# Kernel tuning notes

Hardware: AMD Instinct MI355X
Metric: run time of the kernel (lower is better)

## Reference

```python
import jax, jax.numpy as jnp
import numpy as np

D_MODEL, N_HEADS, D_K, D_V, D_FF, N_LAYERS = 512, 8, 64, 64, 2048, 6
NEG = -1e9
EPS = 1e-5


def layernorm(x):
    # nn.LayerNorm(d_model) created fresh each call: weight=1, bias=0
    mu = jnp.mean(x, axis=-1, keepdims=True)
    var = jnp.var(x, axis=-1, keepdims=True)
    return (x - mu) * jax.lax.rsqrt(var + EPS)


def sinusoidal_pe(seq_len, d_model, dtype=jnp.float32):
    pos = np.arange(seq_len)[:, None].astype(np.float64)
    div = np.exp(np.arange(0, d_model, 2).astype(np.float64) * (-np.log(10000.0) / d_model))
    pe = np.zeros((seq_len, d_model))
    pe[:, 0::2] = np.sin(pos * div)
    pe[:, 1::2] = np.cos(pos * div)
    return jnp.asarray(pe, dtype=dtype)


def mha(q_in, k_in, v_in, mask, Wq, Wk, Wv, Wo):
    # q_in: [B,Lq,D]; k_in/v_in: [B,Lk,D]; mask: [B,Lq,Lk] bool (True = masked)
    B, Lq, _ = q_in.shape
    Lk = k_in.shape[1]
    Q = (q_in @ Wq).reshape(B, Lq, N_HEADS, D_K).transpose(0, 2, 1, 3)
    K = (k_in @ Wk).reshape(B, Lk, N_HEADS, D_K).transpose(0, 2, 1, 3)
    V = (v_in @ Wv).reshape(B, Lk, N_HEADS, D_V).transpose(0, 2, 1, 3)
    scores = jnp.einsum('bhqd,bhkd->bhqk', Q, K) / jnp.sqrt(jnp.asarray(D_K, q_in.dtype))
    scores = jnp.where(mask[:, None, :, :], jnp.asarray(NEG, scores.dtype), scores)
    attn = jax.nn.softmax(scores, axis=-1)
    ctx = jnp.einsum('bhqk,bhkd->bhqd', attn, V)
    ctx = ctx.transpose(0, 2, 1, 3).reshape(B, Lq, N_HEADS * D_V)
    return layernorm(ctx @ Wo + q_in)


def setup_inputs() -> dict:
    key = jax.random.key(0)
    ks = jax.random.split(key, 16)
    B, T, S, V = 8, 1024, 1024, 32000
    s = 0.02
    inp = {
        'dec_inputs': jax.random.randint(ks[0], (B, T), 0, V),
        'enc_inputs': jax.random.randint(ks[1], (B, S), 0, V),
        'enc_outputs': jax.random.normal(ks[2], (B, S, D_MODEL), jnp.float32),
        'emb': jax.random.normal(ks[3], (V, D_MODEL), jnp.float32) * s,
        'Wq_self': jax.random.normal(ks[4], (N_LAYERS, D_MODEL, N_HEADS * D_K), jnp.float32) * s,
        'Wk_self': jax.random.normal(ks[5], (N_LAYERS, D_MODEL, N_HEADS * D_K), jnp.float32) * s,
        'Wv_self': jax.random.normal(ks[6], (N_LAYERS, D_MODEL, N_HEADS * D_V), jnp.float32) * s,
        'Wo_self': jax.random.normal(ks[7], (N_LAYERS, N_HEADS * D_V, D_MODEL), jnp.float32) * s,
        'Wq_cross': jax.random.normal(ks[8], (N_LAYERS, D_MODEL, N_HEADS * D_K), jnp.float32) * s,
        'Wk_cross': jax.random.normal(ks[9], (N_LAYERS, D_MODEL, N_HEADS * D_K), jnp.float32) * s,
        'Wv_cross': jax.random.normal(ks[10], (N_LAYERS, D_MODEL, N_HEADS * D_V), jnp.float32) * s,
        'Wo_cross': jax.random.normal(ks[11], (N_LAYERS, N_HEADS * D_V, D_MODEL), jnp.float32) * s,
        'W1': jax.random.normal(ks[12], (N_LAYERS, D_MODEL, D_FF), jnp.float32) * s,
        'W2': jax.random.normal(ks[13], (N_LAYERS, D_FF, D_MODEL), jnp.float32) * s,
    }
    return inp


def reference(dec_inputs, enc_inputs, enc_outputs, emb, Wq_self, Wk_self, Wv_self, Wo_self,
              Wq_cross, Wk_cross, Wv_cross, Wo_cross, W1, W2):
    B, T = dec_inputs.shape
    S = enc_inputs.shape[1]
    # embedding with padding_idx=0 (row 0 forced to zero)
    emb_eff = emb.at[0].set(0.0)
    x = emb_eff[dec_inputs] + sinusoidal_pe(T, D_MODEL, emb.dtype)[None, :, :]
    # masks: True = masked
    pad_self = (dec_inputs == 0)[:, None, :]                       # [B,1,T]
    causal = jnp.triu(jnp.ones((T, T), bool), k=1)[None, :, :]     # [1,T,T]
    self_mask = pad_self | causal                                  # [B,T,T]
    enc_mask = jnp.broadcast_to((enc_inputs == 0)[:, None, :], (B, T, S))

    def layer(x, p):
        wqs, wks, wvs, wos, wqc, wkc, wvc, woc, w1, w2 = p
        x = mha(x, x, x, self_mask, wqs, wks, wvs, wos)
        x = mha(x, enc_outputs, enc_outputs, enc_mask, wqc, wkc, wvc, woc)
        h = jax.nn.relu(x @ w1) @ w2
        return layernorm(h + x), None

    params = (Wq_self, Wk_self, Wv_self, Wo_self, Wq_cross, Wk_cross, Wv_cross, Wo_cross, W1, W2)
    x, _ = jax.lax.scan(layer, x, params)
    return x
```

## Files before the change

kernel.cpp:

```cpp
#include <hip/hip_runtime.h>
#include <hip/hip_bf16.h>

#define DMODEL 512
#define NH     8
#define DHEAD  64
#define DFF    2048
#define NLAYER 6
#define BB     8
#define TT     1024
#define NTOK   (BB*TT)
#define ACTE   ((size_t)NTOK*DMODEL)

#define QSCALE 0.18033688011112042f

typedef __bf16  bf16x8  __attribute__((ext_vector_type(8)));
typedef float   float4v __attribute__((ext_vector_type(4)));
typedef short   short4v __attribute__((ext_vector_type(4)));
typedef short   short8v __attribute__((ext_vector_type(8)));

__device__ __forceinline__ unsigned short f2bf(float f) {
    __hip_bfloat16 h = __float2bfloat16(f);
    return *reinterpret_cast<unsigned short*>(&h);
}

__device__ __forceinline__ float exp2_fast(float x) {
    float r;
    asm("v_exp_f32 %0, %1\n\ts_nop 0" : "=v"(r) : "v"(x));
    return r;
}

__device__ __forceinline__ void gl_lds16(const void* g, void* l) {
    __builtin_amdgcn_global_load_lds((const __attribute__((address_space(1))) void*)g,
                                     (__attribute__((address_space(3))) void*)l, 16, 0, 0);
}

struct Tr8Args {
    const float* src[8];
    unsigned short* dst[8];
    int dstL[8];
    int rowOff[8];
};
__global__ __launch_bounds__(256) void transpose8_kernel(Tr8Args a)
{
    __shared__ float tile[64][65];
    const int type = blockIdx.z / 6, lyr = blockIdx.z % 6;
    const float* src = a.src[type] + (size_t)lyr * 512 * 512;
    unsigned short* dst = a.dst[type] + (size_t)lyr * a.dstL[type];
    const int rowOff = a.rowOff[type];
    const int k0 = blockIdx.x * 64, n0 = blockIdx.y * 64;
    const int tid = threadIdx.x;
#pragma unroll
    for (int rep = 0; rep < 16; ++rep) {
        int idx = rep * 256 + tid;
        int r = idx >> 6, c = idx & 63;
        tile[r][c] = src[(size_t)(k0 + r) * 512 + n0 + c];
    }
    __syncthreads();
#pragma unroll
    for (int rep = 0; rep < 16; ++rep) {
        int idx = rep * 256 + tid;
        int r = idx >> 6, c = idx & 63;
        dst[(size_t)(rowOff + n0 + r) * 512 + k0 + c] = f2bf(tile[c][r]);
    }
}

__global__ __launch_bounds__(256) void transpose_conv_kernel(
    const float* __restrict__ W, unsigned short* __restrict__ Wt, int K, int N,
    size_t dstL, int rowOff)
{
    __shared__ float tile[64][65];
    const float* src = W + (size_t)blockIdx.z * K * N;
    unsigned short* dst = Wt + (size_t)blockIdx.z * dstL;
    const int k0 = blockIdx.x * 64, n0 = blockIdx.y * 64;
    const int tid = threadIdx.x;
#pragma unroll
    for (int rep = 0; rep < 16; ++rep) {
        int idx = rep * 256 + tid;
        int r = idx >> 6, c = idx & 63;
        tile[r][c] = src[(size_t)(k0 + r) * N + n0 + c];
    }
    __syncthreads();
#pragma unroll
    for (int rep = 0; rep < 16; ++rep) {
        int idx = rep * 256 + tid;
        int r = idx >> 6, c = idx & 63;
        dst[(size_t)(rowOff + n0 + r) * K + k0 + c] = f2bf(tile[c][r]);
    }
}

__global__ __launch_bounds__(256) void conv_bf16_kernel(
    const float* __restrict__ in, unsigned short* __restrict__ o)
{
    int i = (blockIdx.x * 256 + threadIdx.x) * 4;
    float4v v = *(const float4v*)(in + i);
    short4v w;
    w[0] = (short)f2bf(v[0]); w[1] = (short)f2bf(v[1]);
    w[2] = (short)f2bf(v[2]); w[3] = (short)f2bf(v[3]);
    *(short4v*)(o + i) = w;
}

__global__ __launch_bounds__(256) void embed_kernel(
    const int* __restrict__ dec, const float* __restrict__ emb,
    unsigned short* __restrict__ xb)
{
    const int row = blockIdx.x;
    const int t = row & (TT - 1);
    const int tid = threadIdx.x;
    const int tok = dec[row];
#pragma unroll
    for (int rep = 0; rep < 2; ++rep) {
        int c = tid + rep * 256;
        float e = (tok != 0) ? emb[(size_t)tok * DMODEL + c] : 0.f;
        int j = c >> 1;
        float freq = __expf(-(float)(2 * j) * (9.210340371976184f / 512.f));
        float ang = (float)t * freq;
        float pe = (c & 1) ? cosf(ang) : sinf(ang);
        xb[(size_t)row * DMODEL + c] = f2bf(e + pe);
    }
}

__global__ __launch_bounds__(256) void add_ln2(
    const float* __restrict__ t, unsigned short* __restrict__ xb,
    float* __restrict__ xout)
{
    const int lane = threadIdx.x & 63;
    const int row = blockIdx.x * 4 + (threadIdx.x >> 6);
    const size_t idx = (size_t)row * DMODEL + lane * 8;
    float4v t0 = *(const float4v*)(t + idx);
    float4v t1 = *(const float4v*)(t + idx + 4);
    float4v u0 = *(const float4v*)(t + ACTE + idx);
    float4v u1 = *(const float4v*)(t + ACTE + idx + 4);
    bf16x8 rb = *(const bf16x8*)(xb + idx);
    float v[8];
#pragma unroll
    for (int k = 0; k < 4; ++k) {
        v[k] = t0[k] + u0[k] + (float)rb[k];
        v[4 + k] = t1[k] + u1[k] + (float)rb[4 + k];
    }
    float s = 0.f, sq = 0.f;
#pragma unroll
    for (int k = 0; k < 8; ++k) { s += v[k]; sq += v[k] * v[k]; }
#pragma unroll
    for (int o = 1; o < 64; o <<= 1) { s += __shfl_xor(s, o); sq += __shfl_xor(sq, o); }
    float mu = s * (1.f / 512.f);
    float var = sq * (1.f / 512.f) - mu * mu;
    float rstd = rsqrtf(var + 1e-5f);
    if (xout) {
        float4v y0, y1;
#pragma unroll
        for (int k = 0; k < 4; ++k) { y0[k] = (v[k] - mu) * rstd; y1[k] = (v[4 + k] - mu) * rstd; }
        *(float4v*)(xout + idx) = y0;
        *(float4v*)(xout + idx + 4) = y1;
    } else {
        short8v w;
#pragma unroll
        for (int k = 0; k < 8; ++k) w[k] = (short)f2bf((v[k] - mu) * rstd);
        *(short8v*)(xb + idx) = w;
    }
}

template <int EPI, int SPLITK = 1>
__global__ __launch_bounds__(256) void gemm_bt(
    const unsigned short* __restrict__ A,
    const unsigned short* __restrict__ Bt,
    float* __restrict__ Cf,
    unsigned short* __restrict__ Cb,
    int M, int N, int K)
{
    __shared__ __attribute__((aligned(16))) short As[128 * 32];
    __shared__ __attribute__((aligned(16))) short Bs[128 * 32];
    const int tid = threadIdx.x;
    const int lane = tid & 63, wv = tid >> 6;
    const int quad = lane >> 4, l15 = lane & 15;
    const int m0 = blockIdx.x * 128, n0 = blockIdx.y * 128;
    const int wm = wv & 1, wn = wv >> 1;

    float4v acc[4][4];
#pragma unroll
    for (int i = 0; i < 4; ++i)
#pragma unroll
        for (int j = 0; j < 4; ++j) acc[i][j] = (float4v){0.f, 0.f, 0.f, 0.f};

    const int Kc = K / SPLITK;
    const int kbeg = (SPLITK > 1) ? (int)blockIdx.z * Kc : 0;
    for (int k0 = kbeg; k0 < kbeg + Kc; k0 += 32) {
#pragma unroll
        for (int i = 0; i < 2; ++i) {
            const int inst = wv * 2 + i;
            const int row = inst * 16 + (lane >> 2);
            const int cb = (lane & 3) ^ ((row >> 1) & 3);
            gl_lds16(A + (size_t)(m0 + row) * K + k0 + cb * 8, (char*)As + inst * 1024);
            gl_lds16(Bt + (size_t)(n0 + row) * K + k0 + cb * 8, (char*)Bs + inst * 1024);
        }
        __syncthreads();
        bf16x8 a[4], b[4];
#pragma unroll
        for (int i = 0; i < 4; ++i) {
            const int r = wm * 64 + i * 16 + l15;
            const int st = quad ^ ((r >> 1) & 3);
            a[i] = *(const bf16x8*)&As[r * 32 + st * 8];
        }
#pragma unroll
        for (int j = 0; j < 4; ++j) {
            const int r = wn * 64 + j * 16 + l15;
            const int st = quad ^ ((r >> 1) & 3);
            b[j] = *(const bf16x8*)&Bs[r * 32 + st * 8];
        }
#pragma unroll
        for (int i = 0; i < 4; ++i)
#pragma unroll
            for (int j = 0; j < 4; ++j)
                acc[i][j] = __builtin_amdgcn_mfma_f32_16x16x32_bf16(a[i], b[j], acc[i][j], 0, 0, 0);
        __syncthreads();
    }

    const size_t zoff = (SPLITK > 1) ? (size_t)blockIdx.z * ACTE : 0;
#pragma unroll
    for (int i = 0; i < 4; ++i) {
        const int row_base = m0 + wm * 64 + i * 16 + quad * 4;
#pragma unroll
        for (int j = 0; j < 4; ++j) {
            const int col = n0 + wn * 64 + j * 16 + l15;
#pragma unroll
            for (int r = 0; r < 4; ++r) {
                const int row = row_base + r;
                const float v = acc[i][j][r];
                if (EPI == 0) {
                    Cf[zoff + (size_t)row * N + col] = v;
                } else if (EPI == 1) {
                    Cb[(size_t)row * N + col] = f2bf(fmaxf(v, 0.f));
                } else if (EPI == 2) {
                    const int which = col >> 9;
                    const float sc = (which == 0) ? QSCALE : 1.f;
                    const int b_ = row >> 10, t = row & (TT - 1);
                    const int h = (col >> 6) & 7, d = col & 63;
                    Cb[(size_t)which * ACTE + (((size_t)(b_ * NH + h)) * TT + t) * DHEAD + d] = f2bf(v * sc);
                } else {
                    const int layer = col >> 10, which = (col >> 9) & 1;
                    const int b_ = row >> 10, t = row & (TT - 1);
                    const int h = (col >> 6) & 7, d = col & 63;
                    Cb[(size_t)(layer * 2 + which) * ACTE +
                       (((size_t)(b_ * NH + h)) * TT + t) * DHEAD + d] = f2bf(v);
                }
            }
        }
    }
}

template <bool CAUSAL>
__global__ __launch_bounds__(256, 2) void attn_kernel(
    const unsigned short* __restrict__ Q,
    const unsigned short* __restrict__ Kb,
    const unsigned short* __restrict__ Vb,
    const int* __restrict__ tokens,
    unsigned short* __restrict__ ctx)
{
    __shared__ __attribute__((aligned(16))) short Ks[2][64 * 64];
    __shared__ __attribute__((aligned(16))) short Vt[2][64 * 64];
    __shared__ __attribute__((aligned(16))) short Pl[2][4][16 * 72];
    __shared__ __attribute__((aligned(16))) float alph[2][4][16];

    const int tid = threadIdx.x, lane = tid & 63, wv = tid >> 6;
    const int quad = lane >> 4, l15 = lane & 15;
    const int p = blockIdx.x;
    const int bh = blockIdx.y;
    const int b = bh >> 3, h = bh & 7;
    const size_t kvbase = (size_t)bh * TT * DHEAD;

    const int qt0 = p;
    const int qt1 = CAUSAL ? (15 - p) : (p + 8);
    const int qg0 = qt0 * 64 + wv * 16 + l15;
    const int qg1 = qt1 * 64 + wv * 16 + l15;

    const bf16x8 qa0 = *(const bf16x8*)&Q[kvbase + (size_t)qg0 * DHEAD + quad * 8];
    const bf16x8 qa1 = *(const bf16x8*)&Q[kvbase + (size_t)qg0 * DHEAD + 32 + quad * 8];
    const bf16x8 qb0 = *(const bf16x8*)&Q[kvbase + (size_t)qg1 * DHEAD + quad * 8];
    const bf16x8 qb1 = *(const bf16x8*)&Q[kvbase + (size_t)qg1 * DHEAD + 32 + quad * 8];

    float4v O0[4], O1[4];
#pragma unroll
    for (int j = 0; j < 4; ++j) { O0[j] = (float4v){0.f,0.f,0.f,0.f}; O1[j] = (float4v){0.f,0.f,0.f,0.f}; }
    float m0_ = -INFINITY, l0_ = 0.f, m1_ = -INFINITY, l1_ = 0.f;

    const int key0 = (lane & 31) * 2;
    const int d0 = (lane >> 5) * 8 + wv * 16;
    auto stageK = [&](int kt_, int buf) {
#pragma unroll
        for (int i = 0; i < 2; ++i) {
            const int inst = wv * 2 + i;
            const int row = inst * 8 + (lane >> 3);
            const int cb = (lane & 7) ^ (row & 7);
            gl_lds16(Kb + kvbase + (size_t)(kt_ * 64 + row) * DHEAD + cb * 8,
                     (char*)Ks[buf] + inst * 1024);
        }
    };
    auto loadV = [&](int kt_, short8v& r0, short8v& r1) {
        const unsigned short* vp = Vb + kvbase + (size_t)(kt_ * 64 + key0) * DHEAD + d0;
        r0 = *(const short8v*)vp;
        r1 = *(const short8v*)(vp + DHEAD);
    };
    auto writeV = [&](int buf, const short8v& r0, const short8v& r1) {
        const int kc = key0 >> 3, ko = key0 & 7;
#pragma unroll
        for (int j = 0; j < 8; ++j) {
            const int d = d0 + j;
            unsigned pk = (unsigned)(unsigned short)r0[j] |
                          ((unsigned)(unsigned short)r1[j] << 16);
            *(unsigned*)&Vt[buf][d * 64 + ((kc ^ (d & 7)) << 3) + ko] = pk;
        }
    };

    int kt = 0;
    bf16x8 kf[4][2], vf[4][2];

    auto process = [&](int ch, const bf16x8& qf0, const bf16x8& qf1, int qg,
                       float& m, float& l, float4v* O, unsigned long long kbits) {
        float4v st[4];
#pragma unroll
        for (int i = 0; i < 4; ++i) {
            float4v z = (float4v){0.f, 0.f, 0.f, 0.f};
            z = __builtin_amdgcn_mfma_f32_16x16x32_bf16(kf[i][0], qf0, z, 0, 0, 0);
            z = __builtin_amdgcn_mfma_f32_16x16x32_bf16(kf[i][1], qf1, z, 0, 0, 0);
            st[i] = z;
        }
        unsigned long long mask = kbits;
        if (CAUSAL && kt * 64 + 63 > qg) {
            const int qcol = qg & 63;
            mask |= (qcol == 63) ? 0ull : (~0ull << (qcol + 1));
        }
        float sv[16], smax = -INFINITY;
#pragma unroll
        for (int i = 0; i < 4; ++i)
#pragma unroll
            for (int r = 0; r < 4; ++r) {
                const int kl = i * 16 + quad * 4 + r;
                float s = ((mask >> kl) & 1ull) ? -1e9f : st[i][r];
                sv[i * 4 + r] = s;
                smax = fmaxf(smax, s);
            }
        smax = fmaxf(smax, __shfl_xor(smax, 16));
        smax = fmaxf(smax, __shfl_xor(smax, 32));
        const float mnew = fmaxf(m, smax);
        const float alpha = exp2_fast(m - mnew);
        float tsum = 0.f;
#pragma unroll
        for (int i = 0; i < 16; ++i) { float pv = exp2_fast(sv[i] - mnew); sv[i] = pv; tsum += pv; }
        tsum += __shfl_xor(tsum, 16);
        tsum += __shfl_xor(tsum, 32);
        l = l * alpha + tsum;
        m = mnew;
#pragma unroll
        for (int i = 0; i < 4; ++i) {
            short4v pw;
#pragma unroll
            for (int r = 0; r < 4; ++r) pw[r] = (short)f2bf(sv[i * 4 + r]);
            *(short4v*)&Pl[ch][wv][l15 * 72 + i * 16 + quad * 4] = pw;
        }
        if (lane < 16) alph[ch][wv][lane] = alpha;
        const float4v aw = *(const float4v*)&alph[ch][wv][quad * 4];
        const bf16x8 p0 = *(const bf16x8*)&Pl[ch][wv][l15 * 72 + quad * 8];
        const bf16x8 p1 = *(const bf16x8*)&Pl[ch][wv][l15 * 72 + 32 + quad * 8];
#pragma unroll
        for (int j = 0; j < 4; ++j) {
            float4v o = O[j] * aw;
            o = __builtin_amdgcn_mfma_f32_16x16x32_bf16(p0, vf[j][0], o, 0, 0, 0);
            o = __builtin_amdgcn_mfma_f32_16x16x32_bf16(p1, vf[j][1], o, 0, 0, 0);
            O[j] = o;
        }
    };

    const int nkt = CAUSAL ? (qt1 + 1) : 16;

    stageK(0, 0);
    {
        short8v v0a, v0b;
        loadV(0, v0a, v0b);
        writeV(0, v0a, v0b);
    }
    int tok_cur = tokens[(size_t)b * TT + lane];
    __syncthreads();

    short8v vn0, vn1;
    int tok_next = 0;
    for (kt = 0; kt < nkt; ++kt) {
        const int cur = kt & 1, nxt = cur ^ 1;
        const bool more = (kt + 1 < nkt);
        if (more) {
            stageK(kt + 1, nxt);
            loadV(kt + 1, vn0, vn1);
            tok_next = tokens[(size_t)b * TT + (kt + 1) * 64 + lane];
        }
        const unsigned long long kbits = __ballot(tok_cur == 0);

#pragma unroll
        for (int i = 0; i < 4; ++i) {
            const int row = i * 16 + l15;
            const int s0 = quad ^ (row & 7);
            const int s1 = (4 + quad) ^ (row & 7);
            kf[i][0] = *(const bf16x8*)&Ks[cur][row * 64 + s0 * 8];
            kf[i][1] = *(const bf16x8*)&Ks[cur][row * 64 + s1 * 8];
            vf[i][0] = *(const bf16x8*)&Vt[cur][row * 64 + s0 * 8];
            vf[i][1] = *(const bf16x8*)&Vt[cur][row * 64 + s1 * 8];
        }

        if (!CAUSAL || kt <= qt0) process(0, qa0, qa1, qg0, m0_, l0_, O0, kbits);
        process(1, qb0, qb1, qg1, m1_, l1_, O1, kbits);

        if (more) {
            writeV(nxt, vn0, vn1);
            tok_cur = tok_next;
        }
        __syncthreads();
    }

    auto finalize = [&](int ch, float l, float4v* O, int qt) {
        if (lane < 16) alph[ch][wv][lane] = l;
        const float4v lw = *(const float4v*)&alph[ch][wv][quad * 4];
#pragma unroll
        for (int j = 0; j < 4; ++j)
#pragma unroll
            for (int r = 0; r < 4; ++r) {
                const int qrow = qt * 64 + wv * 16 + quad * 4 + r;
                ctx[((size_t)b * TT + qrow) * DMODEL + h * DHEAD + j * 16 + l15] =
                    f2bf(O[j][r] / lw[r]);
            }
    };
    finalize(0, l0_, O0, qt0);
    finalize(1, l1_, O1, qt1);
}

extern "C" void kernel_launch(void* const* d_in, const int* in_sizes, int n_in,
                              void* d_out, int out_size, void* d_ws, size_t ws_size,
                              hipStream_t stream)
{
    const int* dec = (const int*)d_in[0];
    const int* enc = (const int*)d_in[1];
    const float* enc_out = (const float*)d_in[2];
    const float* emb = (const float*)d_in[3];
    const float* Wq_s = (const float*)d_in[4];
    const float* Wk_s = (const float*)d_in[5];
    const float* Wv_s = (const float*)d_in[6];
    const float* Wo_s = (const float*)d_in[7];
    const float* Wq_c = (const float*)d_in[8];
    const float* Wk_c = (const float*)d_in[9];
    const float* Wv_c = (const float*)d_in[10];
    const float* Wo_c = (const float*)d_in[11];
    const float* W1 = (const float*)d_in[12];
    const float* W2 = (const float*)d_in[13];
    float* out = (float*)d_out;

    char* p = (char*)d_ws;
    auto carve = [&](size_t bytes) -> char* {
        char* r = p;
        p += (bytes + 255) & ~(size_t)255;
        return r;
    };
    unsigned short* xb   = (unsigned short*)carve(ACTE * 2);
    float* tmp1          = (float*)carve(2 * ACTE * 4);
    unsigned short* qkvb = (unsigned short*)carve(3 * ACTE * 2);
    unsigned short* ctxb = (unsigned short*)carve(ACTE * 2);
    unsigned short* encb = (unsigned short*)carve(ACTE * 2);
    unsigned short* h1   = (unsigned short*)carve((size_t)NTOK * DFF * 2);
    unsigned short* wqkvT = (unsigned short*)carve((size_t)NLAYER * 1536 * 512 * 2);
    unsigned short* woT   = (unsigned short*)carve((size_t)NLAYER * 512 * 512 * 2);
    unsigned short* wqcT  = (unsigned short*)carve((size_t)NLAYER * 512 * 512 * 2);
    unsigned short* wkvcT = (unsigned short*)carve((size_t)NLAYER * 1024 * 512 * 2);
    unsigned short* wocT  = (unsigned short*)carve((size_t)NLAYER * 512 * 512 * 2);
    unsigned short* w1T   = (unsigned short*)carve((size_t)NLAYER * 2048 * 512 * 2);
    unsigned short* w2T   = (unsigned short*)carve((size_t)NLAYER * 512 * 2048 * 2);
    const size_t used = (size_t)(p - (char*)d_ws);
    const bool pre = (used + 12 * ACTE * 2 + 256) <= ws_size;
    unsigned short* KVc = pre ? (unsigned short*)carve(12 * ACTE * 2) : nullptr;

    Tr8Args ta;
    ta.src[0] = Wq_s; ta.dst[0] = wqkvT; ta.dstL[0] = 1536 * 512; ta.rowOff[0] = 0;
    ta.src[1] = Wk_s; ta.dst[1] = wqkvT; ta.dstL[1] = 1536 * 512; ta.rowOff[1] = 512;
    ta.src[2] = Wv_s; ta.dst[2] = wqkvT; ta.dstL[2] = 1536 * 512; ta.rowOff[2] = 1024;
    ta.src[3] = Wo_s; ta.dst[3] = woT;   ta.dstL[3] = 512 * 512;  ta.rowOff[3] = 0;
    ta.src[4] = Wq_c; ta.dst[4] = wqcT;  ta.dstL[4] = 512 * 512;  ta.rowOff[4] = 0;
    ta.src[5] = Wk_c; ta.dst[5] = wkvcT; ta.dstL[5] = 1024 * 512; ta.rowOff[5] = 0;
    ta.src[6] = Wv_c; ta.dst[6] = wkvcT; ta.dstL[6] = 1024 * 512; ta.rowOff[6] = 512;
    ta.src[7] = Wo_c; ta.dst[7] = wocT;  ta.dstL[7] = 512 * 512;  ta.rowOff[7] = 0;
    transpose8_kernel<<<dim3(8, 8, 48), 256, 0, stream>>>(ta);
    transpose_conv_kernel<<<dim3(8, 32, NLAYER), 256, 0, stream>>>(W1, w1T, 512, 2048, (size_t)2048 * 512, 0);
    transpose_conv_kernel<<<dim3(32, 8, NLAYER), 256, 0, stream>>>(W2, w2T, 2048, 512, (size_t)512 * 2048, 0);
    conv_bf16_kernel<<<(int)(ACTE / 1024), 256, 0, stream>>>(enc_out, encb);
    embed_kernel<<<NTOK, 256, 0, stream>>>(dec, emb, xb);

    if (pre)
        gemm_bt<3><<<dim3(64, 48), 256, 0, stream>>>(encb, wkvcT, nullptr, KVc, NTOK, 6144, 512);

    for (int lyr = 0; lyr < NLAYER; ++lyr) {
        const unsigned short* wqkv = wqkvT + (size_t)lyr * 1536 * 512;
        const unsigned short* wo   = woT + (size_t)lyr * 512 * 512;
        const unsigned short* wqc  = wqcT + (size_t)lyr * 512 * 512;
        const unsigned short* wkvc = wkvcT + (size_t)lyr * 1024 * 512;
        const unsigned short* woc  = wocT + (size_t)lyr * 512 * 512;
        const unsigned short* w1   = w1T + (size_t)lyr * 2048 * 512;
        const unsigned short* w2   = w2T + (size_t)lyr * 512 * 2048;

        gemm_bt<2><<<dim3(64, 12), 256, 0, stream>>>(xb, wqkv, nullptr, qkvb, NTOK, 1536, 512);
        attn_kernel<true><<<dim3(8, BB * NH), 256, 0, stream>>>(
            qkvb, qkvb + ACTE, qkvb + 2 * ACTE, dec, ctxb);
        gemm_bt<0, 2><<<dim3(64, 4, 2), 256, 0, stream>>>(ctxb, wo, tmp1, nullptr, NTOK, 512, 512);
        add_ln2<<<NTOK / 4, 256, 0, stream>>>(tmp1, xb, nullptr);

        gemm_bt<2><<<dim3(64, 4), 256, 0, stream>>>(xb, wqc, nullptr, qkvb, NTOK, 512, 512);
        const unsigned short* Kc;
        if (pre) {
            Kc = KVc + (size_t)lyr * 2 * ACTE;
        } else {
            gemm_bt<2><<<dim3(64, 8), 256, 0, stream>>>(encb, wkvc, nullptr, qkvb + ACTE, NTOK, 1024, 512);
            Kc = qkvb + ACTE;
        }
        attn_kernel<false><<<dim3(8, BB * NH), 256, 0, stream>>>(
            qkvb, Kc, Kc + ACTE, enc, ctxb);
        gemm_bt<0, 2><<<dim3(64, 4, 2), 256, 0, stream>>>(ctxb, woc, tmp1, nullptr, NTOK, 512, 512);
        add_ln2<<<NTOK / 4, 256, 0, stream>>>(tmp1, xb, nullptr);

        gemm_bt<1><<<dim3(64, 16), 256, 0, stream>>>(xb, w1, nullptr, h1, NTOK, 2048, 512);
        gemm_bt<0, 2><<<dim3(64, 4, 2), 256, 0, stream>>>(h1, w2, tmp1, nullptr, NTOK, 512, 2048);
        add_ln2<<<NTOK / 4, 256, 0, stream>>>(tmp1, xb, (lyr == NLAYER - 1) ? out : nullptr);
    }
    (void)in_sizes; (void)n_in; (void)out_size;
}
```

Baseline: 1.647 ms.

## Add lazy softmax rescaling, MFMA priority hints, and swapped attention grid order

The attention kernel now skips the running-max update and O rescale unless some lane's new max exceeds the old one by more than a threshold, as in FA4-style lazy rescaling. It also raises wave priority around the MFMA blocks, widens the P LDS stride to 80, and replaces the final division with a reciprocal multiply. The grid is transposed so that batch-head varies fastest across blocks. These changes are meant to cut exp and rescale ALU work and to change scheduling and cache locality. In exchange they add a wave-wide vote and bound the overflow risk by the threshold.

Result: faster. 1.610 ms (-2.2%).

```diff
diff --git a/kernel.cpp b/kernel.cpp
--- a/kernel.cpp
+++ b/kernel.cpp
@@ -13,6 +13,10 @@
 
 #define QSCALE 0.18033688011112042f
 
+#define RESCALE_THR 8.0f
+
+#define PST 80
+
 typedef __bf16  bf16x8  __attribute__((ext_vector_type(8)));
 typedef float   float4v __attribute__((ext_vector_type(4)));
 typedef short   short4v __attribute__((ext_vector_type(4)));
@@ -21,12 +25,6 @@
 __device__ __forceinline__ unsigned short f2bf(float f) {
     __hip_bfloat16 h = __float2bfloat16(f);
     return *reinterpret_cast<unsigned short*>(&h);
-}
-
-__device__ __forceinline__ float exp2_fast(float x) {
-    float r;
-    asm("v_exp_f32 %0, %1\n\ts_nop 0" : "=v"(r) : "v"(x));
-    return r;
 }
 
 __device__ __forceinline__ void gl_lds16(const void* g, void* l) {
@@ -257,13 +255,13 @@
 {
     __shared__ __attribute__((aligned(16))) short Ks[2][64 * 64];
     __shared__ __attribute__((aligned(16))) short Vt[2][64 * 64];
-    __shared__ __attribute__((aligned(16))) short Pl[2][4][16 * 72];
+    __shared__ __attribute__((aligned(16))) short Pl[2][4][16 * PST];
     __shared__ __attribute__((aligned(16))) float alph[2][4][16];
 
     const int tid = threadIdx.x, lane = tid & 63, wv = tid >> 6;
     const int quad = lane >> 4, l15 = lane & 15;
-    const int p = blockIdx.x;
-    const int bh = blockIdx.y;
+    const int p = blockIdx.y;
+    const int bh = blockIdx.x;
     const int b = bh >> 3, h = bh & 7;
     const size_t kvbase = (size_t)bh * TT * DHEAD;
 
@@ -316,6 +314,7 @@
     auto process = [&](int ch, const bf16x8& qf0, const bf16x8& qf1, int qg,
                        float& m, float& l, float4v* O, unsigned long long kbits) {
         float4v st[4];
+        __builtin_amdgcn_s_setprio(1);
 #pragma unroll
         for (int i = 0; i < 4; ++i) {
             float4v z = (float4v){0.f, 0.f, 0.f, 0.f};
@@ -323,6 +322,7 @@
             z = __builtin_amdgcn_mfma_f32_16x16x32_bf16(kf[i][1], qf1, z, 0, 0, 0);
             st[i] = z;
         }
+        __builtin_amdgcn_s_setprio(0);
         unsigned long long mask = kbits;
         if (CAUSAL && kt * 64 + 63 > qg) {
             const int qcol = qg & 63;
@@ -340,33 +340,45 @@
             }
         smax = fmaxf(smax, __shfl_xor(smax, 16));
         smax = fmaxf(smax, __shfl_xor(smax, 32));
-        const float mnew = fmaxf(m, smax);
-        const float alpha = exp2_fast(m - mnew);
+        const bool resc = !__all(smax - m <= RESCALE_THR);
+        const float mnew = resc ? fmaxf(m, smax) : m;
         float tsum = 0.f;
 #pragma unroll
-        for (int i = 0; i < 16; ++i) { float pv = exp2_fast(sv[i] - mnew); sv[i] = pv; tsum += pv; }
+        for (int i = 0; i < 16; ++i) {
+            float pv = __builtin_amdgcn_exp2f(sv[i] - mnew);
+            sv[i] = pv; tsum += pv;
+        }
         tsum += __shfl_xor(tsum, 16);
         tsum += __shfl_xor(tsum, 32);
-        l = l * alpha + tsum;
-        m = mnew;
 #pragma unroll
         for (int i = 0; i < 4; ++i) {
             short4v pw;
 #pragma unroll
             for (int r = 0; r < 4; ++r) pw[r] = (short)f2bf(sv[i * 4 + r]);
-            *(short4v*)&Pl[ch][wv][l15 * 72 + i * 16 + quad * 4] = pw;
-        }
-        if (lane < 16) alph[ch][wv][lane] = alpha;
-        const float4v aw = *(const float4v*)&alph[ch][wv][quad * 4];
-        const bf16x8 p0 = *(const bf16x8*)&Pl[ch][wv][l15 * 72 + quad * 8];
-        const bf16x8 p1 = *(const bf16x8*)&Pl[ch][wv][l15 * 72 + 32 + quad * 8];
+            *(short4v*)&Pl[ch][wv][l15 * PST + i * 16 + quad * 4] = pw;
+        }
+        if (resc) {
+            const float alpha = __builtin_amdgcn_exp2f(m - mnew);
+            l = l * alpha + tsum;
+            m = mnew;
+            if (lane < 16) alph[ch][wv][lane] = alpha;
+            const float4v aw = *(const float4v*)&alph[ch][wv][quad * 4];
+#pragma unroll
+            for (int j = 0; j < 4; ++j) O[j] = O[j] * aw;
+        } else {
+            l += tsum;
+        }
+        const bf16x8 p0 = *(const bf16x8*)&Pl[ch][wv][l15 * PST + quad * 8];
+        const bf16x8 p1 = *(const bf16x8*)&Pl[ch][wv][l15 * PST + 32 + quad * 8];
+        __builtin_amdgcn_s_setprio(1);
 #pragma unroll
         for (int j = 0; j < 4; ++j) {
-            float4v o = O[j] * aw;
+            float4v o = O[j];
             o = __builtin_amdgcn_mfma_f32_16x16x32_bf16(p0, vf[j][0], o, 0, 0, 0);
             o = __builtin_amdgcn_mfma_f32_16x16x32_bf16(p1, vf[j][1], o, 0, 0, 0);
             O[j] = o;
         }
+        __builtin_amdgcn_s_setprio(0);
     };
 
     const int nkt = CAUSAL ? (qt1 + 1) : 16;
@@ -416,13 +428,16 @@
     auto finalize = [&](int ch, float l, float4v* O, int qt) {
         if (lane < 16) alph[ch][wv][lane] = l;
         const float4v lw = *(const float4v*)&alph[ch][wv][quad * 4];
+        float rl[4];
+#pragma unroll
+        for (int r = 0; r < 4; ++r) rl[r] = __builtin_amdgcn_rcpf(lw[r]);
 #pragma unroll
         for (int j = 0; j < 4; ++j)
 #pragma unroll
             for (int r = 0; r < 4; ++r) {
                 const int qrow = qt * 64 + wv * 16 + quad * 4 + r;
                 ctx[((size_t)b * TT + qrow) * DMODEL + h * DHEAD + j * 16 + l15] =
-                    f2bf(O[j][r] / lw[r]);
+                    f2bf(O[j][r] * rl[r]);
             }
     };
     finalize(0, l0_, O0, qt0);
@@ -500,7 +515,7 @@
         const unsigned short* w2   = w2T + (size_t)lyr * 512 * 2048;
 
         gemm_bt<2><<<dim3(64, 12), 256, 0, stream>>>(xb, wqkv, nullptr, qkvb, NTOK, 1536, 512);
-        attn_kernel<true><<<dim3(8, BB * NH), 256, 0, stream>>>(
+        attn_kernel<true><<<dim3(BB * NH, 8), 256, 0, stream>>>(
             qkvb, qkvb + ACTE, qkvb + 2 * ACTE, dec, ctxb);
         gemm_bt<0, 2><<<dim3(64, 4, 2), 256, 0, stream>>>(ctxb, wo, tmp1, nullptr, NTOK, 512, 512);
         add_ln2<<<NTOK / 4, 256, 0, stream>>>(tmp1, xb, nullptr);
@@ -513,7 +528,7 @@
             gemm_bt<2><<<dim3(64, 8), 256, 0, stream>>>(encb, wkvc, nullptr, qkvb + ACTE, NTOK, 1024, 512);
             Kc = qkvb + ACTE;
         }
-        attn_kernel<false><<<dim3(8, BB * NH), 256, 0, stream>>>(
+        attn_kernel<false><<<dim3(BB * NH, 8), 256, 0, stream>>>(
             qkvb, Kc, Kc + ACTE, enc, ctxb);
         gemm_bt<0, 2><<<dim3(64, 4, 2), 256, 0, stream>>>(ctxb, woc, tmp1, nullptr, NTOK, 512, 512);
         add_ln2<<<NTOK / 4, 256, 0, stream>>>(tmp1, xb, nullptr);
```
